# Performance work log

Hardware: AMD Instinct MI355X
Metric: run time of the kernel (lower is better)

## Reference

```python
import jax, jax.numpy as jnp
import numpy as np


def setup_inputs() -> dict:
    key = jax.random.key(0)
    k1, k2 = jax.random.split(key)
    querry_emb = jax.random.normal(k1, (4096, 1024), dtype=jnp.float32)
    traj_emb = jax.random.normal(k2, (8192, 1024), dtype=jnp.float32)
    return {"querry_emb": querry_emb, "traj_emb": traj_emb}


def reference(querry_emb, traj_emb):
    # Cosine-similarity score: (Q K^T) / (|q| outer |k|)  -> [Nq, Nk]
    q_norm = jnp.sqrt(jnp.sum(querry_emb * querry_emb, axis=1))  # [Nq]
    k_norm = jnp.sqrt(jnp.sum(traj_emb * traj_emb, axis=1))      # [Nk]
    score = jnp.einsum('qd,kd->qk', querry_emb, traj_emb) / (q_norm[:, None] * k_norm[None, :])
    # Softmax over key axis (torch dim=1 on [Nq, Nk])
    atten = jax.nn.softmax(score, axis=1)
    # Context: weighted sum of values (traj_emb)
    context = jnp.einsum('qk,kd->qd', atten, traj_emb)
    return context
```

## Files before the change

### kernel.cpp

```cpp
#include <hip/hip_runtime.h>

#define NQ 4096
#define NK 8192
#define DIM 1024

typedef __attribute__((ext_vector_type(8))) short short8;
typedef __attribute__((ext_vector_type(4))) float floatx4;
typedef unsigned int u32;
typedef __attribute__((address_space(3))) u32 lds_u32;
typedef __attribute__((address_space(1))) const u32 glb_u32;

__device__ __forceinline__ void gload_lds16(const void* g, void* l) {
    __builtin_amdgcn_global_load_lds((glb_u32*)g, (lds_u32*)l, 16, 0, 0);
}

__device__ __forceinline__ unsigned short f32_bf16(float f) {
    unsigned int u = __float_as_uint(f);
    u += 0x7fff + ((u >> 16) & 1);
    return (unsigned short)(u >> 16);
}

__global__ void prep_q_zero(const float* __restrict__ Q,
                            unsigned short* __restrict__ Qb,
                            float* __restrict__ inv_qn,
                            float* __restrict__ lsum,
                            float* __restrict__ out_zero) {
    int wave = threadIdx.x >> 6;
    int lane = threadIdx.x & 63;
    int row  = blockIdx.x * 4 + wave;
    const float* r = Q + (size_t)row * DIM;
    float s = 0.f;
#pragma unroll
    for (int c = 0; c < 4; ++c) {
        float4 f = *(const float4*)(r + c * 256 + lane * 4);
        s += f.x * f.x + f.y * f.y + f.z * f.z + f.w * f.w;
        ushort4 b;
        b.x = f32_bf16(f.x); b.y = f32_bf16(f.y);
        b.z = f32_bf16(f.z); b.w = f32_bf16(f.w);
        *(ushort4*)(Qb + (size_t)row * DIM + c * 256 + lane * 4) = b;
    }
#pragma unroll
    for (int off = 32; off > 0; off >>= 1) s += __shfl_xor(s, off);
    if (lane == 0) inv_qn[row] = 1.0f / sqrtf(s);

    float4 z = make_float4(0.f, 0.f, 0.f, 0.f);
    if (out_zero) {
#pragma unroll
        for (int c = 0; c < 4; ++c)
            *(float4*)(out_zero + (size_t)blockIdx.x * 4096 + c * 1024 + threadIdx.x * 4) = z;
    }
    if (blockIdx.x < 4)
        *(float4*)(lsum + blockIdx.x * 1024 + threadIdx.x * 4) = z;
}

__global__ void prep_norm_cvt(const float* __restrict__ src,
                              unsigned short* __restrict__ dst,
                              float* __restrict__ inv_norm) {
    int wave = threadIdx.x >> 6;
    int lane = threadIdx.x & 63;
    int row  = blockIdx.x * 4 + wave;
    const float* r = src + (size_t)row * DIM;
    float s = 0.f;
#pragma unroll
    for (int c = 0; c < 4; ++c) {
        float4 f = *(const float4*)(r + c * 256 + lane * 4);
        s += f.x * f.x + f.y * f.y + f.z * f.z + f.w * f.w;
        ushort4 b;
        b.x = f32_bf16(f.x); b.y = f32_bf16(f.y);
        b.z = f32_bf16(f.z); b.w = f32_bf16(f.w);
        *(ushort4*)(dst + (size_t)row * DIM + c * 256 + lane * 4) = b;
    }
#pragma unroll
    for (int off = 32; off > 0; off >>= 1) s += __shfl_xor(s, off);
    if (lane == 0) inv_norm[row] = 1.0f / sqrtf(s);
}

__global__ void transpose_cvt(const float* __restrict__ K,
                              unsigned short* __restrict__ Kt) {
    __shared__ float t[64][65];
    int kn0 = blockIdx.x * 64, d0 = blockIdx.y * 64;
    int tid = threadIdx.x;
    int r  = tid >> 4;
    int c4 = (tid & 15) * 4;
#pragma unroll
    for (int s = 0; s < 4; ++s) {
        int kk = s * 16 + r;
        float4 f = *(const float4*)(K + (size_t)(kn0 + kk) * DIM + d0 + c4);
        t[kk][c4 + 0] = f.x; t[kk][c4 + 1] = f.y;
        t[kk][c4 + 2] = f.z; t[kk][c4 + 3] = f.w;
    }
    __syncthreads();
#pragma unroll
    for (int s = 0; s < 4; ++s) {
        int dd = s * 16 + r;
        ushort4 b;
        b.x = f32_bf16(t[c4 + 0][dd]);
        b.y = f32_bf16(t[c4 + 1][dd]);
        b.z = f32_bf16(t[c4 + 2][dd]);
        b.w = f32_bf16(t[c4 + 3][dd]);
        *(ushort4*)(Kt + (size_t)(d0 + dd) * NK + kn0 + c4) = b;
    }
}

__global__ __launch_bounds__(512, 2) void score_gemm(
        const unsigned short* __restrict__ Qb,
        const unsigned short* __restrict__ Kb,
        const float* __restrict__ inv_qn,
        const float* __restrict__ inv_kn,
        unsigned short* __restrict__ P,
        float* __restrict__ lsum) {
    __shared__ __align__(16) unsigned short A_lds[2][2][256 * 32];
    __shared__ __align__(16) unsigned short B_lds[2][2][256 * 32];

    int bid = blockIdx.x;
    int swz = (bid & 7) * 64 + (bid >> 3);
    int q0  = (swz & 15) * 256;
    int n0  = (swz >> 4) * 256;

    int tid  = threadIdx.x;
    int wave = tid >> 6, lane = tid & 63;
    int wm = wave >> 2, wn = wave & 3;
    int quad = lane >> 4, l16 = lane & 15;
    int rcol = (quad ^ ((l16 >> 1) & 3)) * 8;

    int schunk = ((tid & 3) ^ ((tid >> 3) & 3)) * 8;
    const unsigned short* gA = Qb + (size_t)(q0 + (tid >> 2)) * DIM + schunk;
    const unsigned short* gB = Kb + (size_t)(n0 + (tid >> 2)) * DIM + schunk;

#define STG_A(t1, pan)                                                \
    do {                                                              \
        const unsigned short* _g = gA + (t1) * 64 + (pan) * 32;       \
        unsigned short* _l = &A_lds[(t1) & 1][pan][wave * 512];       \
        gload_lds16(_g, _l);                                          \
        gload_lds16(_g + (size_t)128 * DIM, _l + 4096);               \
    } while (0)
#define STG_B(t1, pan)                                                \
    do {                                                              \
        const unsigned short* _g = gB + (t1) * 64 + (pan) * 32;       \
        unsigned short* _l = &B_lds[(t1) & 1][pan][wave * 512];       \
        gload_lds16(_g, _l);                                          \
        gload_lds16(_g + (size_t)128 * DIM, _l + 4096);               \
    } while (0)

    floatx4 acc[8][4];
#pragma unroll
    for (int i = 0; i < 8; ++i)
#pragma unroll
        for (int j = 0; j < 4; ++j) acc[i][j] = (floatx4)(0.0f);

    short8 a[4][2], bA[2][2], bB[2][2];

    STG_A(0, 0); STG_A(0, 1); STG_B(0, 0); STG_B(0, 1);
    asm volatile("s_waitcnt vmcnt(0)" ::: "memory");
    __syncthreads();

    for (int t = 0; t < 16; ++t) {
        const unsigned short* A0 = &A_lds[t & 1][0][0];
        const unsigned short* A1 = &A_lds[t & 1][1][0];
        const unsigned short* B0 = &B_lds[t & 1][0][0];
        const unsigned short* B1 = &B_lds[t & 1][1][0];
        const int ar = (wm * 128 + l16) * 32 + rcol;
        const int br = (wn * 64 + l16) * 32 + rcol;

#pragma unroll
        for (int mi = 0; mi < 4; ++mi) {
            a[mi][0] = *(const short8*)&A0[ar + mi * 512];
            a[mi][1] = *(const short8*)&A1[ar + mi * 512];
        }
#pragma unroll
        for (int nj = 0; nj < 2; ++nj) {
            bA[nj][0] = *(const short8*)&B0[br + nj * 512];
            bA[nj][1] = *(const short8*)&B1[br + nj * 512];
        }
        if (t < 15) { STG_A(t + 1, 0); STG_A(t + 1, 1); }
        __builtin_amdgcn_s_barrier();
        __builtin_amdgcn_s_setprio(1);
#pragma unroll
        for (int mi = 0; mi < 4; ++mi)
#pragma unroll
            for (int nj = 0; nj < 2; ++nj) {
                acc[mi][nj] = __builtin_amdgcn_mfma_f32_16x16x32_bf16(bA[nj][0], a[mi][0], acc[mi][nj], 0, 0, 0);
                acc[mi][nj] = __builtin_amdgcn_mfma_f32_16x16x32_bf16(bA[nj][1], a[mi][1], acc[mi][nj], 0, 0, 0);
            }
        __builtin_amdgcn_s_setprio(0);
        __builtin_amdgcn_s_barrier();

#pragma unroll
        for (int nj = 0; nj < 2; ++nj) {
            bB[nj][0] = *(const short8*)&B0[br + 1024 + nj * 512];
            bB[nj][1] = *(const short8*)&B1[br + 1024 + nj * 512];
        }
        if (t < 15) { STG_B(t + 1, 0); STG_B(t + 1, 1); }
        __builtin_amdgcn_s_barrier();
        __builtin_amdgcn_s_setprio(1);
#pragma unroll
        for (int mi = 0; mi < 4; ++mi)
#pragma unroll
            for (int nj = 0; nj < 2; ++nj) {
                acc[mi][2 + nj] = __builtin_amdgcn_mfma_f32_16x16x32_bf16(bB[nj][0], a[mi][0], acc[mi][2 + nj], 0, 0, 0);
                acc[mi][2 + nj] = __builtin_amdgcn_mfma_f32_16x16x32_bf16(bB[nj][1], a[mi][1], acc[mi][2 + nj], 0, 0, 0);
            }
        __builtin_amdgcn_s_setprio(0);
        __builtin_amdgcn_s_barrier();

#pragma unroll
        for (int mi = 0; mi < 4; ++mi) {
            a[mi][0] = *(const short8*)&A0[ar + 2048 + mi * 512];
            a[mi][1] = *(const short8*)&A1[ar + 2048 + mi * 512];
        }
        __builtin_amdgcn_s_barrier();
        __builtin_amdgcn_s_setprio(1);
#pragma unroll
        for (int mi = 0; mi < 4; ++mi)
#pragma unroll
            for (int nj = 0; nj < 2; ++nj) {
                acc[4 + mi][2 + nj] = __builtin_amdgcn_mfma_f32_16x16x32_bf16(bB[nj][0], a[mi][0], acc[4 + mi][2 + nj], 0, 0, 0);
                acc[4 + mi][2 + nj] = __builtin_amdgcn_mfma_f32_16x16x32_bf16(bB[nj][1], a[mi][1], acc[4 + mi][2 + nj], 0, 0, 0);
            }
        __builtin_amdgcn_s_setprio(0);
        __builtin_amdgcn_s_barrier();

        __builtin_amdgcn_s_setprio(1);
#pragma unroll
        for (int mi = 0; mi < 4; ++mi)
#pragma unroll
            for (int nj = 0; nj < 2; ++nj) {
                acc[4 + mi][nj] = __builtin_amdgcn_mfma_f32_16x16x32_bf16(bA[nj][0], a[mi][0], acc[4 + mi][nj], 0, 0, 0);
                acc[4 + mi][nj] = __builtin_amdgcn_mfma_f32_16x16x32_bf16(bA[nj][1], a[mi][1], acc[4 + mi][nj], 0, 0, 0);
            }
        __builtin_amdgcn_s_setprio(0);
        if (t < 15) asm volatile("s_waitcnt vmcnt(0)" ::: "memory");
        __builtin_amdgcn_s_barrier();
    }
#undef STG_A
#undef STG_B

#pragma unroll
    for (int i = 0; i < 8; ++i) {
        int qrow = q0 + wm * 128 + i * 16 + l16;
        float iqn = inv_qn[qrow];
        float rs = 0.f;
#pragma unroll
        for (int j = 0; j < 4; ++j) {
            int ncol = n0 + wn * 64 + j * 16 + quad * 4;
            float4 ik = *(const float4*)&inv_kn[ncol];
            float p0 = __expf(acc[i][j][0] * iqn * ik.x);
            float p1 = __expf(acc[i][j][1] * iqn * ik.y);
            float p2 = __expf(acc[i][j][2] * iqn * ik.z);
            float p3 = __expf(acc[i][j][3] * iqn * ik.w);
            ushort4 pb;
            pb.x = f32_bf16(p0); pb.y = f32_bf16(p1);
            pb.z = f32_bf16(p2); pb.w = f32_bf16(p3);
            *(ushort4*)&P[(size_t)qrow * NK + ncol] = pb;
            rs += p0 + p1 + p2 + p3;
        }
        rs += __shfl_xor(rs, 16);
        rs += __shfl_xor(rs, 32);
        if (quad == 0) atomicAdd(&lsum[qrow], rs);
    }
}

__global__ __launch_bounds__(512, 2) void ctx_gemm_st(
        const unsigned short* __restrict__ P,
        const unsigned short* __restrict__ Kt,
        float* __restrict__ part) {
    __shared__ __align__(16) unsigned short A_lds[2][2][256 * 32];
    __shared__ __align__(16) unsigned short B_lds[2][2][256 * 32];

    int bid = blockIdx.x;
    int swz = (bid & 7) * 32 + (bid >> 3);
    int z  = swz >> 6;
    int y  = (swz >> 2) & 15;
    int x  = swz & 3;
    int q0 = y * 256;
    int d0 = x * 256;
    int kbase = z * (NK / 4);

    int tid  = threadIdx.x;
    int wave = tid >> 6, lane = tid & 63;
    int wm = wave >> 2, wn = wave & 3;
    int quad = lane >> 4, l16 = lane & 15;
    int rcol = (quad ^ ((l16 >> 1) & 3)) * 8;

    int schunk = ((tid & 3) ^ ((tid >> 3) & 3)) * 8;
    const unsigned short* gA = P  + (size_t)(q0 + (tid >> 2)) * NK + kbase + schunk;
    const unsigned short* gB = Kt + (size_t)(d0 + (tid >> 2)) * NK + kbase + schunk;

#define STG_A(t1, pan)                                                \
    do {                                                              \
        const unsigned short* _g = gA + (t1) * 64 + (pan) * 32;       \
        unsigned short* _l = &A_lds[(t1) & 1][pan][wave * 512];       \
        gload_lds16(_g, _l);                                          \
        gload_lds16(_g + (size_t)128 * NK, _l + 4096);                \
    } while (0)
#define STG_B(t1, pan)                                                \
    do {                                                              \
        const unsigned short* _g = gB + (t1) * 64 + (pan) * 32;       \
        unsigned short* _l = &B_lds[(t1) & 1][pan][wave * 512];       \
        gload_lds16(_g, _l);                                          \
        gload_lds16(_g + (size_t)128 * NK, _l + 4096);                \
    } while (0)

    floatx4 acc[8][4];
#pragma unroll
    for (int i = 0; i < 8; ++i)
#pragma unroll
        for (int j = 0; j < 4; ++j) acc[i][j] = (floatx4)(0.0f);

    short8 a[4][2], bA[2][2], bB[2][2];

    STG_A(0, 0); STG_A(0, 1); STG_B(0, 0); STG_B(0, 1);
    asm volatile("s_waitcnt vmcnt(0)" ::: "memory");
    __syncthreads();

    const int NT = (NK / 4) / 64;
    for (int t = 0; t < NT; ++t) {
        const unsigned short* A0 = &A_lds[t & 1][0][0];
        const unsigned short* A1 = &A_lds[t & 1][1][0];
        const unsigned short* B0 = &B_lds[t & 1][0][0];
        const unsigned short* B1 = &B_lds[t & 1][1][0];
        const int ar = (wm * 128 + l16) * 32 + rcol;
        const int br = (wn * 64 + l16) * 32 + rcol;

#pragma unroll
        for (int mi = 0; mi < 4; ++mi) {
            a[mi][0] = *(const short8*)&A0[ar + mi * 512];
            a[mi][1] = *(const short8*)&A1[ar + mi * 512];
        }
#pragma unroll
        for (int nj = 0; nj < 2; ++nj) {
            bA[nj][0] = *(const short8*)&B0[br + nj * 512];
            bA[nj][1] = *(const short8*)&B1[br + nj * 512];
        }
        if (t < NT - 1) { STG_A(t + 1, 0); STG_A(t + 1, 1); }
        __builtin_amdgcn_s_barrier();
        __builtin_amdgcn_s_setprio(1);
#pragma unroll
        for (int mi = 0; mi < 4; ++mi)
#pragma unroll
            for (int nj = 0; nj < 2; ++nj) {
                acc[mi][nj] = __builtin_amdgcn_mfma_f32_16x16x32_bf16(bA[nj][0], a[mi][0], acc[mi][nj], 0, 0, 0);
                acc[mi][nj] = __builtin_amdgcn_mfma_f32_16x16x32_bf16(bA[nj][1], a[mi][1], acc[mi][nj], 0, 0, 0);
            }
        __builtin_amdgcn_s_setprio(0);
        __builtin_amdgcn_s_barrier();

#pragma unroll
        for (int nj = 0; nj < 2; ++nj) {
            bB[nj][0] = *(const short8*)&B0[br + 1024 + nj * 512];
            bB[nj][1] = *(const short8*)&B1[br + 1024 + nj * 512];
        }
        if (t < NT - 1) { STG_B(t + 1, 0); STG_B(t + 1, 1); }
        __builtin_amdgcn_s_barrier();
        __builtin_amdgcn_s_setprio(1);
#pragma unroll
        for (int mi = 0; mi < 4; ++mi)
#pragma unroll
            for (int nj = 0; nj < 2; ++nj) {
                acc[mi][2 + nj] = __builtin_amdgcn_mfma_f32_16x16x32_bf16(bB[nj][0], a[mi][0], acc[mi][2 + nj], 0, 0, 0);
                acc[mi][2 + nj] = __builtin_amdgcn_mfma_f32_16x16x32_bf16(bB[nj][1], a[mi][1], acc[mi][2 + nj], 0, 0, 0);
            }
        __builtin_amdgcn_s_setprio(0);
        __builtin_amdgcn_s_barrier();

#pragma unroll
        for (int mi = 0; mi < 4; ++mi) {
            a[mi][0] = *(const short8*)&A0[ar + 2048 + mi * 512];
            a[mi][1] = *(const short8*)&A1[ar + 2048 + mi * 512];
        }
        __builtin_amdgcn_s_barrier();
        __builtin_amdgcn_s_setprio(1);
#pragma unroll
        for (int mi = 0; mi < 4; ++mi)
#pragma unroll
            for (int nj = 0; nj < 2; ++nj) {
                acc[4 + mi][2 + nj] = __builtin_amdgcn_mfma_f32_16x16x32_bf16(bB[nj][0], a[mi][0], acc[4 + mi][2 + nj], 0, 0, 0);
                acc[4 + mi][2 + nj] = __builtin_amdgcn_mfma_f32_16x16x32_bf16(bB[nj][1], a[mi][1], acc[4 + mi][2 + nj], 0, 0, 0);
            }
        __builtin_amdgcn_s_setprio(0);
        __builtin_amdgcn_s_barrier();

        __builtin_amdgcn_s_setprio(1);
#pragma unroll
        for (int mi = 0; mi < 4; ++mi)
#pragma unroll
            for (int nj = 0; nj < 2; ++nj) {
                acc[4 + mi][nj] = __builtin_amdgcn_mfma_f32_16x16x32_bf16(bA[nj][0], a[mi][0], acc[4 + mi][nj], 0, 0, 0);
                acc[4 + mi][nj] = __builtin_amdgcn_mfma_f32_16x16x32_bf16(bA[nj][1], a[mi][1], acc[4 + mi][nj], 0, 0, 0);
            }
        __builtin_amdgcn_s_setprio(0);
        if (t < NT - 1) asm volatile("s_waitcnt vmcnt(0)" ::: "memory");
        __builtin_amdgcn_s_barrier();
    }
#undef STG_A
#undef STG_B

    float* pslice = part + (size_t)z * NQ * DIM;
#pragma unroll
    for (int i = 0; i < 8; ++i) {
        int qrow = q0 + wm * 128 + i * 16 + l16;
#pragma unroll
        for (int j = 0; j < 4; ++j) {
            int dcol = d0 + wn * 64 + j * 16 + quad * 4;
            float4 v;
            v.x = acc[i][j][0]; v.y = acc[i][j][1];
            v.z = acc[i][j][2]; v.w = acc[i][j][3];
            *(float4*)&pslice[(size_t)qrow * DIM + dcol] = v;
        }
    }
}

__global__ void reduce_out(const float* __restrict__ part,
                           const float* __restrict__ lsum,
                           float* __restrict__ out) {
    size_t idx = ((size_t)blockIdx.x * 256 + threadIdx.x) * 4;
    int q = (int)(idx >> 10);
    float inv = 1.0f / lsum[q];
    const size_t S = (size_t)NQ * DIM;
    float4 s0 = *(const float4*)(part + idx);
    float4 s1 = *(const float4*)(part + S + idx);
    float4 s2 = *(const float4*)(part + 2 * S + idx);
    float4 s3 = *(const float4*)(part + 3 * S + idx);
    float4 o;
    o.x = (s0.x + s1.x + s2.x + s3.x) * inv;
    o.y = (s0.y + s1.y + s2.y + s3.y) * inv;
    o.z = (s0.z + s1.z + s2.z + s3.z) * inv;
    o.w = (s0.w + s1.w + s2.w + s3.w) * inv;
    *(float4*)(out + idx) = o;
}

__global__ void ctx_gemm(const unsigned short* __restrict__ P,
                         const unsigned short* __restrict__ Kt,
                         const float* __restrict__ lsum,
                         float* __restrict__ out) {
    __shared__ __align__(16) unsigned short As[128 * 32];
    __shared__ __align__(16) unsigned short Bs[128 * 32];
    int id = blockIdx.x;
    int r8 = id & 7;
    int t  = id >> 3;
    int x  = t & 7;
    int g  = ((t >> 3) << 3) | r8;
    int y  = g & 31;
    int z  = g >> 5;
    int q0 = y * 128;
    int d0 = x * 128;
    int kbase = z * (NK / 4);

    int tid = threadIdx.x;
    int wave = tid >> 6, lane = tid & 63;
    int wm = wave >> 1, wn = wave & 1;
    int quad = lane >> 4, l16 = lane & 15;

    int srow   = wave * 32 + (lane >> 2);
    int schunk = (((lane & 3) ^ ((lane >> 3) & 3))) * 8;
    const unsigned short* gA0 = P + (size_t)(q0 + srow) * NK + kbase + schunk;
    const unsigned short* gA1 = gA0 + (size_t)16 * NK;
    const unsigned short* gB0 = Kt + (size_t)(d0 + srow) * NK + kbase + schunk;
    const unsigned short* gB1 = gB0 + (size_t)16 * NK;
    unsigned short* lA0 = As + wave * 32 * 32;
    unsigned short* lA1 = lA0 + 16 * 32;
    unsigned short* lB0 = Bs + wave * 32 * 32;
    unsigned short* lB1 = lB0 + 16 * 32;

    int rcol = (quad ^ ((l16 >> 1) & 3)) * 8;

    floatx4 acc[4][4];
#pragma unroll
    for (int i = 0; i < 4; ++i)
#pragma unroll
        for (int j = 0; j < 4; ++j) acc[i][j] = (floatx4)(0.0f);

    for (int kb = 0; kb < (NK / 4) / 32; ++kb) {
        int k0 = kb * 32;
        __syncthreads();
        gload_lds16(gA0 + k0, lA0);
        gload_lds16(gA1 + k0, lA1);
        gload_lds16(gB0 + k0, lB0);
        gload_lds16(gB1 + k0, lB1);
        __syncthreads();
        short8 a[4], b[4];
#pragma unroll
        for (int i = 0; i < 4; ++i)
            a[i] = *(const short8*)&As[(wm * 64 + i * 16 + l16) * 32 + rcol];
#pragma unroll
        for (int j = 0; j < 4; ++j)
            b[j] = *(const short8*)&Bs[(wn * 64 + j * 16 + l16) * 32 + rcol];
#pragma unroll
        for (int i = 0; i < 4; ++i)
#pragma unroll
            for (int j = 0; j < 4; ++j)
                acc[i][j] = __builtin_amdgcn_mfma_f32_16x16x32_bf16(a[i], b[j], acc[i][j], 0, 0, 0);
    }

#pragma unroll
    for (int i = 0; i < 4; ++i) {
        float invl[4];
#pragma unroll
        for (int r = 0; r < 4; ++r)
            invl[r] = 1.0f / lsum[q0 + wm * 64 + i * 16 + quad * 4 + r];
#pragma unroll
        for (int j = 0; j < 4; ++j) {
#pragma unroll
            for (int r = 0; r < 4; ++r) {
                int qrow = q0 + wm * 64 + i * 16 + quad * 4 + r;
                int dcol = d0 + wn * 64 + j * 16 + l16;
                atomicAdd(&out[(size_t)qrow * DIM + dcol], acc[i][j][r] * invl[r]);
            }
        }
    }
}

__global__ void fused_fallback(const float* __restrict__ Q,
                               const float* __restrict__ K,
                               float* __restrict__ out) {
    int wave = threadIdx.x >> 6, lane = threadIdx.x & 63;
    int q0 = blockIdx.x * 16 + wave * 4;
    float qv[4][16], acc[4][16], iqn[4], ls[4];
#pragma unroll
    for (int r = 0; r < 4; ++r) {
        float s = 0.f;
#pragma unroll
        for (int c = 0; c < 4; ++c) {
            float4 f = *(const float4*)(Q + (size_t)(q0 + r) * DIM + c * 256 + lane * 4);
            qv[r][c * 4 + 0] = f.x; qv[r][c * 4 + 1] = f.y;
            qv[r][c * 4 + 2] = f.z; qv[r][c * 4 + 3] = f.w;
            s += f.x * f.x + f.y * f.y + f.z * f.z + f.w * f.w;
        }
#pragma unroll
        for (int off = 32; off > 0; off >>= 1) s += __shfl_xor(s, off);
        iqn[r] = 1.0f / sqrtf(s);
        ls[r] = 0.f;
#pragma unroll
        for (int t = 0; t < 16; ++t) acc[r][t] = 0.f;
    }
    for (int k = 0; k < NK; ++k) {
        const float* kr = K + (size_t)k * DIM;
        float kv[16], ss = 0.f;
#pragma unroll
        for (int c = 0; c < 4; ++c) {
            float4 f = *(const float4*)(kr + c * 256 + lane * 4);
            kv[c * 4 + 0] = f.x; kv[c * 4 + 1] = f.y;
            kv[c * 4 + 2] = f.z; kv[c * 4 + 3] = f.w;
            ss += f.x * f.x + f.y * f.y + f.z * f.z + f.w * f.w;
        }
        float d0 = 0.f, d1 = 0.f, d2 = 0.f, d3 = 0.f;
#pragma unroll
        for (int t = 0; t < 16; ++t) {
            d0 += qv[0][t] * kv[t]; d1 += qv[1][t] * kv[t];
            d2 += qv[2][t] * kv[t]; d3 += qv[3][t] * kv[t];
        }
#pragma unroll
        for (int off = 32; off > 0; off >>= 1) {
            ss += __shfl_xor(ss, off);
            d0 += __shfl_xor(d0, off); d1 += __shfl_xor(d1, off);
            d2 += __shfl_xor(d2, off); d3 += __shfl_xor(d3, off);
        }
        float ikn = 1.0f / sqrtf(ss);
        float p0 = __expf(d0 * iqn[0] * ikn), p1 = __expf(d1 * iqn[1] * ikn);
        float p2 = __expf(d2 * iqn[2] * ikn), p3 = __expf(d3 * iqn[3] * ikn);
        ls[0] += p0; ls[1] += p1; ls[2] += p2; ls[3] += p3;
#pragma unroll
        for (int t = 0; t < 16; ++t) {
            acc[0][t] += p0 * kv[t]; acc[1][t] += p1 * kv[t];
            acc[2][t] += p2 * kv[t]; acc[3][t] += p3 * kv[t];
        }
    }
#pragma unroll
    for (int r = 0; r < 4; ++r) {
        float inv = 1.0f / ls[r];
#pragma unroll
        for (int c = 0; c < 4; ++c) {
            float4 o;
            o.x = acc[r][c * 4 + 0] * inv; o.y = acc[r][c * 4 + 1] * inv;
            o.z = acc[r][c * 4 + 2] * inv; o.w = acc[r][c * 4 + 3] * inv;
            *(float4*)(out + (size_t)(q0 + r) * DIM + c * 256 + lane * 4) = o;
        }
    }
}

extern "C" void kernel_launch(void* const* d_in, const int* in_sizes, int n_in,
                              void* d_out, int out_size, void* d_ws, size_t ws_size,
                              hipStream_t stream) {
    const float* Q = (const float*)d_in[0];
    const float* K = (const float*)d_in[1];
    float* out = (float*)d_out;
    char* ws = (char*)d_ws;

    const size_t REQ_T1 = ((size_t)152u << 20) + 65536;
    const size_t REQ_T2 = ((size_t)88u << 20) + 65536;

    if (ws_size >= REQ_T1) {
        unsigned short* Kt = (unsigned short*)(ws);
        unsigned short* Qb = (unsigned short*)(ws);
        unsigned short* Kb = (unsigned short*)(ws + (size_t)(8u << 20));
        unsigned short* P  = (unsigned short*)(ws + (size_t)(24u << 20));
        float* part   = (float*)(ws + (size_t)(88u << 20));
        float* inv_qn = (float*)(ws + (size_t)(152u << 20));
        float* inv_kn = (float*)(ws + (size_t)(152u << 20) + 16384);
        float* lsum   = (float*)(ws + (size_t)(152u << 20) + 49152);

        prep_q_zero<<<NQ / 4, 256, 0, stream>>>(Q, Qb, inv_qn, lsum, nullptr);
        prep_norm_cvt<<<NK / 4, 256, 0, stream>>>(K, Kb, inv_kn);
        score_gemm<<<512, 512, 0, stream>>>(Qb, Kb, inv_qn, inv_kn, P, lsum);
        transpose_cvt<<<dim3(NK / 64, DIM / 64), 256, 0, stream>>>(K, Kt);
        ctx_gemm_st<<<256, 512, 0, stream>>>(P, Kt, part);
        reduce_out<<<NQ * DIM / 1024, 256, 0, stream>>>(part, lsum, out);
    } else if (ws_size >= REQ_T2) {
        unsigned short* Kt = (unsigned short*)(ws);
        unsigned short* Qb = (unsigned short*)(ws);
        unsigned short* Kb = (unsigned short*)(ws + (size_t)(8u << 20));
        unsigned short* P  = (unsigned short*)(ws + (size_t)(24u << 20));
        float* inv_qn = (float*)(ws + (size_t)(88u << 20));
        float* inv_kn = (float*)(ws + (size_t)(88u << 20) + 16384);
        float* lsum   = (float*)(ws + (size_t)(88u << 20) + 49152);

        prep_q_zero<<<NQ / 4, 256, 0, stream>>>(Q, Qb, inv_qn, lsum, out);
        prep_norm_cvt<<<NK / 4, 256, 0, stream>>>(K, Kb, inv_kn);
        score_gemm<<<512, 512, 0, stream>>>(Qb, Kb, inv_qn, inv_kn, P, lsum);
        transpose_cvt<<<dim3(NK / 64, DIM / 64), 256, 0, stream>>>(K, Kt);
        ctx_gemm<<<1024, 256, 0, stream>>>(P, Kt, lsum, out);
    } else {
        fused_fallback<<<NQ / 16, 256, 0, stream>>>(Q, K, out);
    }
}
```

Before: 261.3 us.

## Prefetch B tiles two iterations ahead with partial vmcnt waits

Restructures the global-to-LDS staging in both GEMM kernels so B panels load two k-steps ahead while A panels load one step ahead, spread across the four MFMA phases. The end-of-iteration wait becomes vmcnt(4) instead of draining every outstanding load, which keeps loads in flight across iterations and hides more memory latency. It adds an extra barrier per iteration and unrolls the loop by two. It also depends on the B double buffer not being overwritten while it is still being read, which makes the buffer timing harder to get right.

Result: slower. 268.3 us (+2.7%).

```diff
diff --git a/kernel.cpp b/kernel.cpp
--- a/kernel.cpp
+++ b/kernel.cpp
@@ -150,11 +150,14 @@
 
     short8 a[4][2], bA[2][2], bB[2][2];
 
+    const int NT = 16;
     STG_A(0, 0); STG_A(0, 1); STG_B(0, 0); STG_B(0, 1);
-    asm volatile("s_waitcnt vmcnt(0)" ::: "memory");
-    __syncthreads();
-
-    for (int t = 0; t < 16; ++t) {
+    STG_B(1, 0); STG_B(1, 1);
+    asm volatile("s_waitcnt vmcnt(4)" ::: "memory");
+    __builtin_amdgcn_s_barrier();
+
+#pragma unroll 2
+    for (int t = 0; t < NT; ++t) {
         const unsigned short* A0 = &A_lds[t & 1][0][0];
         const unsigned short* A1 = &A_lds[t & 1][1][0];
         const unsigned short* B0 = &B_lds[t & 1][0][0];
@@ -172,7 +175,7 @@
             bA[nj][0] = *(const short8*)&B0[br + nj * 512];
             bA[nj][1] = *(const short8*)&B1[br + nj * 512];
         }
-        if (t < 15) { STG_A(t + 1, 0); STG_A(t + 1, 1); }
+        if (t + 1 < NT) STG_A(t + 1, 0);
         __builtin_amdgcn_s_barrier();
         __builtin_amdgcn_s_setprio(1);
 #pragma unroll
@@ -190,7 +193,7 @@
             bB[nj][0] = *(const short8*)&B0[br + 1024 + nj * 512];
             bB[nj][1] = *(const short8*)&B1[br + 1024 + nj * 512];
         }
-        if (t < 15) { STG_B(t + 1, 0); STG_B(t + 1, 1); }
+        if (t + 1 < NT) STG_A(t + 1, 1);
         __builtin_amdgcn_s_barrier();
         __builtin_amdgcn_s_setprio(1);
 #pragma unroll
@@ -208,6 +211,7 @@
             a[mi][0] = *(const short8*)&A0[ar + 2048 + mi * 512];
             a[mi][1] = *(const short8*)&A1[ar + 2048 + mi * 512];
         }
+        if (t + 2 < NT) STG_B(t + 2, 0);
         __builtin_amdgcn_s_barrier();
         __builtin_amdgcn_s_setprio(1);
 #pragma unroll
@@ -220,6 +224,8 @@
         __builtin_amdgcn_s_setprio(0);
         __builtin_amdgcn_s_barrier();
 
+        if (t + 2 < NT) STG_B(t + 2, 1);
+        __builtin_amdgcn_s_barrier();
         __builtin_amdgcn_s_setprio(1);
 #pragma unroll
         for (int mi = 0; mi < 4; ++mi)
@@ -229,7 +235,11 @@
                 acc[4 + mi][nj] = __builtin_amdgcn_mfma_f32_16x16x32_bf16(bA[nj][1], a[mi][1], acc[4 + mi][nj], 0, 0, 0);
             }
         __builtin_amdgcn_s_setprio(0);
-        if (t < 15) asm volatile("s_waitcnt vmcnt(0)" ::: "memory");
+        if (t + 2 < NT) {
+            asm volatile("s_waitcnt vmcnt(4)" ::: "memory");
+        } else if (t + 1 < NT) {
+            asm volatile("s_waitcnt vmcnt(0)" ::: "memory");
+        }
         __builtin_amdgcn_s_barrier();
     }
 #undef STG_A
@@ -309,11 +319,13 @@
 
     short8 a[4][2], bA[2][2], bB[2][2];
 
+    const int NT = (NK / 4) / 64;
     STG_A(0, 0); STG_A(0, 1); STG_B(0, 0); STG_B(0, 1);
-    asm volatile("s_waitcnt vmcnt(0)" ::: "memory");
-    __syncthreads();
-
-    const int NT = (NK / 4) / 64;
+    STG_B(1, 0); STG_B(1, 1);
+    asm volatile("s_waitcnt vmcnt(4)" ::: "memory");
+    __builtin_amdgcn_s_barrier();
+
+#pragma unroll 2
     for (int t = 0; t < NT; ++t) {
         const unsigned short* A0 = &A_lds[t & 1][0][0];
         const unsigned short* A1 = &A_lds[t & 1][1][0];
@@ -332,7 +344,7 @@
             bA[nj][0] = *(const short8*)&B0[br + nj * 512];
             bA[nj][1] = *(const short8*)&B1[br + nj * 512];
         }
-        if (t < NT - 1) { STG_A(t + 1, 0); STG_A(t + 1, 1); }
+        if (t + 1 < NT) STG_A(t + 1, 0);
         __builtin_amdgcn_s_barrier();
         __builtin_amdgcn_s_setprio(1);
 #pragma unroll
@@ -350,7 +362,7 @@
             bB[nj][0] = *(const short8*)&B0[br + 1024 + nj * 512];
             bB[nj][1] = *(const short8*)&B1[br + 1024 + nj * 512];
         }
-        if (t < NT - 1) { STG_B(t + 1, 0); STG_B(t + 1, 1); }
+        if (t + 1 < NT) STG_A(t + 1, 1);
         __builtin_amdgcn_s_barrier();
         __builtin_amdgcn_s_setprio(1);
 #pragma unroll
@@ -368,6 +380,7 @@
             a[mi][0] = *(const short8*)&A0[ar + 2048 + mi * 512];
             a[mi][1] = *(const short8*)&A1[ar + 2048 + mi * 512];
         }
+        if (t + 2 < NT) STG_B(t + 2, 0);
         __builtin_amdgcn_s_barrier();
         __builtin_amdgcn_s_setprio(1);
 #pragma unroll
@@ -380,6 +393,8 @@
         __builtin_amdgcn_s_setprio(0);
         __builtin_amdgcn_s_barrier();
 
+        if (t + 2 < NT) STG_B(t + 2, 1);
+        __builtin_amdgcn_s_barrier();
         __builtin_amdgcn_s_setprio(1);
 #pragma unroll
         for (int mi = 0; mi < 4; ++mi)
@@ -389,7 +404,11 @@
                 acc[4 + mi][nj] = __builtin_amdgcn_mfma_f32_16x16x32_bf16(bA[nj][1], a[mi][1], acc[4 + mi][nj], 0, 0, 0);
             }
         __builtin_amdgcn_s_setprio(0);
-        if (t < NT - 1) asm volatile("s_waitcnt vmcnt(0)" ::: "memory");
+        if (t + 2 < NT) {
+            asm volatile("s_waitcnt vmcnt(4)" ::: "memory");
+        } else if (t + 1 < NT) {
+            asm volatile("s_waitcnt vmcnt(0)" ::: "memory");
+        }
         __builtin_amdgcn_s_barrier();
     }
 #undef STG_A
```

## Fuse Q/K prep kernels, transpose from bf16 K, store split-K partials as bf16

Applied to the files above, without the earlier changes.

The separate Q and K normalize-and-convert kernels become one launch. The K transpose now reads the already-converted bf16 K instead of the fp32 original, and it runs before score_gemm in its own workspace region. The split-K context partials are written as bf16 instead of fp32, which halves partial write and reduce read traffic. The cost is an extra rounding of the partial sums to bf16 before the final reduction, which lowers output accuracy.

Result: faster. 249.1 us (-4.7%).

```diff
diff --git a/kernel.cpp b/kernel.cpp
--- a/kernel.cpp
+++ b/kernel.cpp
@@ -20,45 +20,30 @@
     return (unsigned short)(u >> 16);
 }
 
-__global__ void prep_q_zero(const float* __restrict__ Q,
-                            unsigned short* __restrict__ Qb,
-                            float* __restrict__ inv_qn,
-                            float* __restrict__ lsum,
-                            float* __restrict__ out_zero) {
+__device__ __forceinline__ float bf16_f32(unsigned short u) {
+    return __uint_as_float((u32)u << 16);
+}
+
+__global__ void prep_all(const float* __restrict__ Q,
+                         const float* __restrict__ K,
+                         unsigned short* __restrict__ Qb,
+                         unsigned short* __restrict__ Kb,
+                         float* __restrict__ inv_qn,
+                         float* __restrict__ inv_kn,
+                         float* __restrict__ lsum,
+                         float* __restrict__ out_zero) {
     int wave = threadIdx.x >> 6;
     int lane = threadIdx.x & 63;
-    int row  = blockIdx.x * 4 + wave;
-    const float* r = Q + (size_t)row * DIM;
-    float s = 0.f;
-#pragma unroll
-    for (int c = 0; c < 4; ++c) {
-        float4 f = *(const float4*)(r + c * 256 + lane * 4);
-        s += f.x * f.x + f.y * f.y + f.z * f.z + f.w * f.w;
-        ushort4 b;
-        b.x = f32_bf16(f.x); b.y = f32_bf16(f.y);
-        b.z = f32_bf16(f.z); b.w = f32_bf16(f.w);
-        *(ushort4*)(Qb + (size_t)row * DIM + c * 256 + lane * 4) = b;
-    }
-#pragma unroll
-    for (int off = 32; off > 0; off >>= 1) s += __shfl_xor(s, off);
-    if (lane == 0) inv_qn[row] = 1.0f / sqrtf(s);
-
-    float4 z = make_float4(0.f, 0.f, 0.f, 0.f);
-    if (out_zero) {
-#pragma unroll
-        for (int c = 0; c < 4; ++c)
-            *(float4*)(out_zero + (size_t)blockIdx.x * 4096 + c * 1024 + threadIdx.x * 4) = z;
-    }
-    if (blockIdx.x < 4)
-        *(float4*)(lsum + blockIdx.x * 1024 + threadIdx.x * 4) = z;
-}
-
-__global__ void prep_norm_cvt(const float* __restrict__ src,
-                              unsigned short* __restrict__ dst,
-                              float* __restrict__ inv_norm) {
-    int wave = threadIdx.x >> 6;
-    int lane = threadIdx.x & 63;
-    int row  = blockIdx.x * 4 + wave;
+    int bid  = blockIdx.x;
+    const float* src;
+    unsigned short* dst;
+    float* invp;
+    int row;
+    if (bid < NQ / 4) {
+        row = bid * 4 + wave; src = Q; dst = Qb; invp = inv_qn;
+    } else {
+        row = (bid - NQ / 4) * 4 + wave; src = K; dst = Kb; invp = inv_kn;
+    }
     const float* r = src + (size_t)row * DIM;
     float s = 0.f;
 #pragma unroll
@@ -72,7 +57,43 @@
     }
 #pragma unroll
     for (int off = 32; off > 0; off >>= 1) s += __shfl_xor(s, off);
-    if (lane == 0) inv_norm[row] = 1.0f / sqrtf(s);
+    if (lane == 0) invp[row] = 1.0f / sqrtf(s);
+
+    if (bid < NQ / 4) {
+        float4 z = make_float4(0.f, 0.f, 0.f, 0.f);
+        if (out_zero) {
+#pragma unroll
+            for (int c = 0; c < 4; ++c)
+                *(float4*)(out_zero + (size_t)bid * 4096 + c * 1024 + threadIdx.x * 4) = z;
+        }
+        if (bid < 4)
+            *(float4*)(lsum + bid * 1024 + threadIdx.x * 4) = z;
+    }
+}
+
+__global__ void transpose_bf16(const unsigned short* __restrict__ Kb,
+                               unsigned short* __restrict__ Kt) {
+    __shared__ unsigned short t[64][66];
+    int kn0 = blockIdx.x * 64, d0 = blockIdx.y * 64;
+    int tid = threadIdx.x;
+    int r  = tid >> 4;
+    int c4 = (tid & 15) * 4;
+#pragma unroll
+    for (int s = 0; s < 4; ++s) {
+        int kk = s * 16 + r;
+        ushort4 v = *(const ushort4*)(Kb + (size_t)(kn0 + kk) * DIM + d0 + c4);
+        t[kk][c4 + 0] = v.x; t[kk][c4 + 1] = v.y;
+        t[kk][c4 + 2] = v.z; t[kk][c4 + 3] = v.w;
+    }
+    __syncthreads();
+#pragma unroll
+    for (int s = 0; s < 4; ++s) {
+        int dd = s * 16 + r;
+        ushort4 b;
+        b.x = t[c4 + 0][dd]; b.y = t[c4 + 1][dd];
+        b.z = t[c4 + 2][dd]; b.w = t[c4 + 3][dd];
+        *(ushort4*)(Kt + (size_t)(d0 + dd) * NK + kn0 + c4) = b;
+    }
 }
 
 __global__ void transpose_cvt(const float* __restrict__ K,
@@ -263,7 +284,7 @@
 __global__ __launch_bounds__(512, 2) void ctx_gemm_st(
         const unsigned short* __restrict__ P,
         const unsigned short* __restrict__ Kt,
-        float* __restrict__ part) {
+        unsigned short* __restrict__ part) {
     __shared__ __align__(16) unsigned short A_lds[2][2][256 * 32];
     __shared__ __align__(16) unsigned short B_lds[2][2][256 * 32];
 
@@ -395,37 +416,37 @@
 #undef STG_A
 #undef STG_B
 
-    float* pslice = part + (size_t)z * NQ * DIM;
+    unsigned short* pslice = part + (size_t)z * NQ * DIM;
 #pragma unroll
     for (int i = 0; i < 8; ++i) {
         int qrow = q0 + wm * 128 + i * 16 + l16;
 #pragma unroll
         for (int j = 0; j < 4; ++j) {
             int dcol = d0 + wn * 64 + j * 16 + quad * 4;
-            float4 v;
-            v.x = acc[i][j][0]; v.y = acc[i][j][1];
-            v.z = acc[i][j][2]; v.w = acc[i][j][3];
-            *(float4*)&pslice[(size_t)qrow * DIM + dcol] = v;
-        }
-    }
-}
-
-__global__ void reduce_out(const float* __restrict__ part,
+            ushort4 v;
+            v.x = f32_bf16(acc[i][j][0]); v.y = f32_bf16(acc[i][j][1]);
+            v.z = f32_bf16(acc[i][j][2]); v.w = f32_bf16(acc[i][j][3]);
+            *(ushort4*)&pslice[(size_t)qrow * DIM + dcol] = v;
+        }
+    }
+}
+
+__global__ void reduce_out(const unsigned short* __restrict__ part,
                            const float* __restrict__ lsum,
                            float* __restrict__ out) {
     size_t idx = ((size_t)blockIdx.x * 256 + threadIdx.x) * 4;
     int q = (int)(idx >> 10);
     float inv = 1.0f / lsum[q];
     const size_t S = (size_t)NQ * DIM;
-    float4 s0 = *(const float4*)(part + idx);
-    float4 s1 = *(const float4*)(part + S + idx);
-    float4 s2 = *(const float4*)(part + 2 * S + idx);
-    float4 s3 = *(const float4*)(part + 3 * S + idx);
+    ushort4 a0 = *(const ushort4*)(part + idx);
+    ushort4 a1 = *(const ushort4*)(part + S + idx);
+    ushort4 a2 = *(const ushort4*)(part + 2 * S + idx);
+    ushort4 a3 = *(const ushort4*)(part + 3 * S + idx);
     float4 o;
-    o.x = (s0.x + s1.x + s2.x + s3.x) * inv;
-    o.y = (s0.y + s1.y + s2.y + s3.y) * inv;
-    o.z = (s0.z + s1.z + s2.z + s3.z) * inv;
-    o.w = (s0.w + s1.w + s2.w + s3.w) * inv;
+    o.x = (bf16_f32(a0.x) + bf16_f32(a1.x) + bf16_f32(a2.x) + bf16_f32(a3.x)) * inv;
+    o.y = (bf16_f32(a0.y) + bf16_f32(a1.y) + bf16_f32(a2.y) + bf16_f32(a3.y)) * inv;
+    o.z = (bf16_f32(a0.z) + bf16_f32(a1.z) + bf16_f32(a2.z) + bf16_f32(a3.z)) * inv;
+    o.w = (bf16_f32(a0.w) + bf16_f32(a1.w) + bf16_f32(a2.w) + bf16_f32(a3.w)) * inv;
     *(float4*)(out + idx) = o;
 }
 
@@ -590,19 +611,18 @@
     const size_t REQ_T2 = ((size_t)88u << 20) + 65536;
 
     if (ws_size >= REQ_T1) {
-        unsigned short* Kt = (unsigned short*)(ws);
         unsigned short* Qb = (unsigned short*)(ws);
         unsigned short* Kb = (unsigned short*)(ws + (size_t)(8u << 20));
         unsigned short* P  = (unsigned short*)(ws + (size_t)(24u << 20));
-        float* part   = (float*)(ws + (size_t)(88u << 20));
+        unsigned short* part = (unsigned short*)(ws + (size_t)(88u << 20));
+        unsigned short* Kt = (unsigned short*)(ws + (size_t)(120u << 20));
         float* inv_qn = (float*)(ws + (size_t)(152u << 20));
         float* inv_kn = (float*)(ws + (size_t)(152u << 20) + 16384);
         float* lsum   = (float*)(ws + (size_t)(152u << 20) + 49152);
 
-        prep_q_zero<<<NQ / 4, 256, 0, stream>>>(Q, Qb, inv_qn, lsum, nullptr);
-        prep_norm_cvt<<<NK / 4, 256, 0, stream>>>(K, Kb, inv_kn);
+        prep_all<<<NQ / 4 + NK / 4, 256, 0, stream>>>(Q, K, Qb, Kb, inv_qn, inv_kn, lsum, nullptr);
+        transpose_bf16<<<dim3(NK / 64, DIM / 64), 256, 0, stream>>>(Kb, Kt);
         score_gemm<<<512, 512, 0, stream>>>(Qb, Kb, inv_qn, inv_kn, P, lsum);
-        transpose_cvt<<<dim3(NK / 64, DIM / 64), 256, 0, stream>>>(K, Kt);
         ctx_gemm_st<<<256, 512, 0, stream>>>(P, Kt, part);
         reduce_out<<<NQ * DIM / 1024, 256, 0, stream>>>(part, lsum, out);
     } else if (ws_size >= REQ_T2) {
@@ -614,8 +634,7 @@
         float* inv_kn = (float*)(ws + (size_t)(88u << 20) + 16384);
         float* lsum   = (float*)(ws + (size_t)(88u << 20) + 49152);
 
-        prep_q_zero<<<NQ / 4, 256, 0, stream>>>(Q, Qb, inv_qn, lsum, out);
-        prep_norm_cvt<<<NK / 4, 256, 0, stream>>>(K, Kb, inv_kn);
+        prep_all<<<NQ / 4 + NK / 4, 256, 0, stream>>>(Q, K, Qb, Kb, inv_qn, inv_kn, lsum, out);
         score_gemm<<<512, 512, 0, stream>>>(Qb, Kb, inv_qn, inv_kn, P, lsum);
         transpose_cvt<<<dim3(NK / 64, DIM / 64), 256, 0, stream>>>(K, Kt);
         ctx_gemm<<<1024, 256, 0, stream>>>(P, Kt, lsum, out);
```
